# Kernel tuning notes

Measured on AMD Instinct MI355X. Metric: run time of the kernel, lower is better.

## Reference

```python
import jax, jax.numpy as jnp
import numpy as np

NUM_EMBEDDINGS = 512
EMBEDDING_DIM = 256
COMMITMENT_COST = 0.25


def setup_inputs() -> dict:
    key = jax.random.key(0)
    k1, k2 = jax.random.split(key)
    z = jax.random.normal(k1, (8, EMBEDDING_DIM, 16, 32, 32), dtype=jnp.float32)
    # codebook initialized uniform(-1/K, 1/K) like the torch module
    e = jax.random.uniform(k2, (NUM_EMBEDDINGS, EMBEDDING_DIM), dtype=jnp.float32,
                           minval=-1.0 / NUM_EMBEDDINGS, maxval=1.0 / NUM_EMBEDDINGS)
    return {"z": z, "e": e}


def reference(z, e):
    B, D, T, h, w = z.shape
    K = e.shape[0]
    # [B,D,T,h,w] -> [N, D]
    z_flat = jnp.transpose(z, (0, 2, 3, 4, 1)).reshape(-1, D)
    # squared L2 distances to codebook: [N, K]
    d = (jnp.sum(z_flat ** 2, axis=1, keepdims=True)
         + jnp.sum(e ** 2, axis=1)
         - 2.0 * z_flat @ e.T)
    idx = jnp.argmin(d, axis=1)                      # [N] int
    z_q_raw = e[idx].reshape(B, T, h, w, D)          # codebook gather
    z_q_raw = jnp.transpose(z_q_raw, (0, 4, 1, 2, 3))  # [B,D,T,h,w]

    commit = jnp.mean((jax.lax.stop_gradient(z_q_raw) - z) ** 2)
    codebk = jnp.mean((z_q_raw - jax.lax.stop_gradient(z)) ** 2)
    vq_loss = codebk + COMMITMENT_COST * commit

    # straight-through estimator
    z_q = z + jax.lax.stop_gradient(z_q_raw - z)

    # perplexity: histogram of code usage (avoids materializing NxK one-hot)
    N = idx.shape[0]
    avg_probs = jnp.zeros((K,), z.dtype).at[idx].add(1.0) / N
    perplexity = jnp.exp(-jnp.sum(avg_probs * jnp.log(avg_probs + 1e-10)))

    return z_q, vq_loss, idx, perplexity
```

## Files before the change

kernel.cpp:

```cpp
#include <hip/hip_runtime.h>
#include <math.h>

#define N_POS     131072
#define DIM       256
#define K_CODES   512
#define S_SPATIAL 16384
#define ZQ_ELEMS  33554432
#define OUT_LOSS  33554432
#define OUT_IDXB  33554433
#define OUT_PERP  (33554433 + 131072)

#define WS_LOSS   0
#define WS_HIST   16
#define WS_E2     2064
#define WS_FIXED  2064

__global__ __launch_bounds__(256) void e2_kernel(const float* __restrict__ e,
                                                 float* __restrict__ e2) {
    int k = blockIdx.x * 256 + threadIdx.x;
    if (k >= K_CODES) return;
    const float* row = e + (size_t)k * DIM;
    float half[2];
#pragma unroll
    for (int h = 0; h < 2; ++h) {
        const float* base = row + h * 128;
        float r[8];
#pragma unroll
        for (int j = 0; j < 8; ++j) {
            float v = base[j];
            r[j] = __fmul_rn(v, v);
        }
        for (int i = 8; i < 128; i += 8) {
#pragma unroll
            for (int j = 0; j < 8; ++j) {
                float v = base[i + j];
                r[j] = __fadd_rn(r[j], __fmul_rn(v, v));
            }
        }
        half[h] = __fadd_rn(__fadd_rn(__fadd_rn(r[0], r[1]), __fadd_rn(r[2], r[3])),
                            __fadd_rn(__fadd_rn(r[4], r[5]), __fadd_rn(r[6], r[7])));
    }
    e2[k] = __fadd_rn(half[0], half[1]);
}

__global__ __launch_bounds__(256) void transpose_e(const float* __restrict__ e,
                                                   float* __restrict__ eTq) {
    int t = blockIdx.x * 256 + threadIdx.x;
    int k = t >> 8;
    int d = t & 255;
    float v = e[t];
    int c = k >> 7;
    int w = (k >> 6) & 1;
    int l = k & 63;
    eTq[(((d << 1) + w) << 8) + (l << 2) + c] = v;
}

__global__ __launch_bounds__(256) void sz_kernel(const float* __restrict__ z,
                                                 float* __restrict__ sz) {
    int n = blockIdx.x * 256 + threadIdx.x;
    int b = n >> 14;
    int s = n & (S_SPATIAL - 1);
    const float* zp = z + (size_t)b * (DIM * S_SPATIAL) + s;
    float half[2];
#pragma unroll
    for (int h = 0; h < 2; ++h) {
        const float* base = zp + (size_t)(h * 128) * S_SPATIAL;
        float r[8];
#pragma unroll
        for (int j = 0; j < 8; ++j) {
            float v = base[(size_t)j * S_SPATIAL];
            r[j] = __fmul_rn(v, v);
        }
        for (int i = 8; i < 128; i += 8) {
#pragma unroll
            for (int j = 0; j < 8; ++j) {
                float v = base[(size_t)(i + j) * S_SPATIAL];
                r[j] = __fadd_rn(r[j], __fmul_rn(v, v));
            }
        }
        half[h] = __fadd_rn(__fadd_rn(__fadd_rn(r[0], r[1]), __fadd_rn(r[2], r[3])),
                            __fadd_rn(__fadd_rn(r[4], r[5]), __fadd_rn(r[6], r[7])));
    }
    sz[n] = __fadd_rn(half[0], half[1]);
}

__global__ __launch_bounds__(128, 4) void pass1_dist(const float* __restrict__ z,
                                                     const float* __restrict__ eTq,
                                                     const float* __restrict__ e2,
                                                     const float* __restrict__ sz,
                                                     float* __restrict__ idxf,
                                                     int* __restrict__ ghist) {
    const int lane = threadIdx.x & 63;
    const int wave = threadIdx.x >> 6;
    const int n0   = blockIdx.x << 4;
    const int b    = n0 >> 14;
    const float* zb = z + (size_t)b * (DIM * S_SPATIAL) + (n0 & (S_SPATIAL - 1));

    __shared__ float zs[DIM][16];
    __shared__ unsigned long long lred[2][16];

    for (int j = threadIdx.x; j < 1024; j += 128) {
        int d  = j >> 2;
        int p4 = (j & 3) << 2;
        float4 v = *(const float4*)(zb + ((size_t)d << 14) + p4);
        *(float4*)(&zs[d][p4]) = v;
    }

    float szv = sz[n0 + (lane & 15)];

    const int kbase = (wave << 6) + lane;
    float se0 = e2[kbase];
    float se1 = e2[kbase + 128];
    float se2 = e2[kbase + 256];
    float se3 = e2[kbase + 384];

    float a0[16], a1[16], a2[16], a3[16];
#pragma unroll
    for (int p = 0; p < 16; ++p) { a0[p] = 0.f; a1[p] = 0.f; a2[p] = 0.f; a3[p] = 0.f; }

    __syncthreads();

    const float* ep = eTq + (size_t)(((wave << 6) + lane) << 2);
#pragma unroll 2
    for (int d = 0; d < DIM; ++d) {
        float4 ev = *(const float4*)(ep + ((size_t)d << 9));
        float zv[16];
        *(float4*)(zv +  0) = *(const float4*)(&zs[d][ 0]);
        *(float4*)(zv +  4) = *(const float4*)(&zs[d][ 4]);
        *(float4*)(zv +  8) = *(const float4*)(&zs[d][ 8]);
        *(float4*)(zv + 12) = *(const float4*)(&zs[d][12]);
#pragma unroll
        for (int p = 0; p < 16; ++p) {
            a0[p] = __fmaf_rn(zv[p], ev.x, a0[p]);
            a1[p] = __fmaf_rn(zv[p], ev.y, a1[p]);
            a2[p] = __fmaf_rn(zv[p], ev.z, a2[p]);
            a3[p] = __fmaf_rn(zv[p], ev.w, a3[p]);
        }
    }

#pragma unroll
    for (int p = 0; p < 16; ++p) {
        float szp = __shfl(szv, p);
        float d0 = __fsub_rn(__fadd_rn(szp, se0), __fmul_rn(2.0f, a0[p]));
        float d1 = __fsub_rn(__fadd_rn(szp, se1), __fmul_rn(2.0f, a1[p]));
        float d2 = __fsub_rn(__fadd_rn(szp, se2), __fmul_rn(2.0f, a2[p]));
        float d3 = __fsub_rn(__fadd_rn(szp, se3), __fmul_rn(2.0f, a3[p]));
        unsigned long long k0 =
            ((unsigned long long)__float_as_uint(d0) << 32) | (unsigned int)(kbase);
        unsigned long long k1 =
            ((unsigned long long)__float_as_uint(d1) << 32) | (unsigned int)(kbase + 128);
        unsigned long long k2 =
            ((unsigned long long)__float_as_uint(d2) << 32) | (unsigned int)(kbase + 256);
        unsigned long long k3 =
            ((unsigned long long)__float_as_uint(d3) << 32) | (unsigned int)(kbase + 384);
        unsigned long long m01 = k1 < k0 ? k1 : k0;
        unsigned long long m23 = k3 < k2 ? k3 : k2;
        unsigned long long kmin = m23 < m01 ? m23 : m01;
#pragma unroll
        for (int off = 32; off; off >>= 1) {
            unsigned long long o = __shfl_xor(kmin, off);
            kmin = o < kmin ? o : kmin;
        }
        if (lane == 0) lred[wave][p] = kmin;
    }
    __syncthreads();
    if (threadIdx.x < 16) {
        int p = threadIdx.x;
        unsigned long long m = lred[0][p] < lred[1][p] ? lred[0][p] : lred[1][p];
        int idx = (int)(unsigned int)(m & 0xffffffffull);
        idxf[n0 + p] = (float)idx;
        atomicAdd(&ghist[idx], 1);
    }
}

__global__ __launch_bounds__(256) void gather_loss(const float* __restrict__ z,
                                                   const float* __restrict__ e,
                                                   const float* __restrict__ idxf,
                                                   float* __restrict__ out,
                                                   double* __restrict__ loss) {
    int t = blockIdx.x * 256 + threadIdx.x;
    int b   = t >> 14;
    int r   = t & 16383;
    int dg  = r >> 12;
    int sp  = (r & 4095) << 2;
    int n0  = (b << 14) + sp;

    int k0 = (int)idxf[n0 + 0];
    int k1 = (int)idxf[n0 + 1];
    int k2 = (int)idxf[n0 + 2];
    int k3 = (int)idxf[n0 + 3];
    const float* e0 = e + (size_t)k0 * DIM;
    const float* e1 = e + (size_t)k1 * DIM;
    const float* e2p = e + (size_t)k2 * DIM;
    const float* e3 = e + (size_t)k3 * DIM;

    const float* zb = z + ((size_t)b * DIM << 14) + sp;
    float* ob = out + ((size_t)b * DIM << 14) + sp;

    double acc = 0.0;
    int dend = dg * 64 + 64;
    for (int d0 = dg * 64; d0 < dend; d0 += 4) {
        float4 ev0 = *(const float4*)(e0 + d0);
        float4 ev1 = *(const float4*)(e1 + d0);
        float4 ev2 = *(const float4*)(e2p + d0);
        float4 ev3 = *(const float4*)(e3 + d0);
#pragma unroll
        for (int dd = 0; dd < 4; ++dd) {
            size_t off = ((size_t)(d0 + dd) << 14);
            float4 zv = *(const float4*)(zb + off);
            float ea = (dd == 0) ? ev0.x : (dd == 1) ? ev0.y : (dd == 2) ? ev0.z : ev0.w;
            float eb_ = (dd == 0) ? ev1.x : (dd == 1) ? ev1.y : (dd == 2) ? ev1.z : ev1.w;
            float ec = (dd == 0) ? ev2.x : (dd == 1) ? ev2.y : (dd == 2) ? ev2.z : ev2.w;
            float ed = (dd == 0) ? ev3.x : (dd == 1) ? ev3.y : (dd == 2) ? ev3.z : ev3.w;
            float d0f = __fsub_rn(ea, zv.x);
            float d1f = __fsub_rn(eb_, zv.y);
            float d2f = __fsub_rn(ec, zv.z);
            float d3f = __fsub_rn(ed, zv.w);
            float4 ov;
            ov.x = __fadd_rn(zv.x, d0f);
            ov.y = __fadd_rn(zv.y, d1f);
            ov.z = __fadd_rn(zv.z, d2f);
            ov.w = __fadd_rn(zv.w, d3f);
            *(float4*)(ob + off) = ov;
            acc += (double)d0f * (double)d0f;
            acc += (double)d1f * (double)d1f;
            acc += (double)d2f * (double)d2f;
            acc += (double)d3f * (double)d3f;
        }
    }
    for (int off = 32; off; off >>= 1) acc += __shfl_down(acc, off);
    __shared__ double red[4];
    if ((threadIdx.x & 63) == 0) red[threadIdx.x >> 6] = acc;
    __syncthreads();
    if (threadIdx.x == 0) {
        double tsum = red[0] + red[1] + red[2] + red[3];
        atomicAdd(loss, tsum);
    }
}

__global__ __launch_bounds__(512) void finalize_kernel(const int* __restrict__ ghist,
                                                       const double* __restrict__ loss,
                                                       float* __restrict__ out) {
    int k = threadIdx.x;
    double p = (double)ghist[k] / (double)N_POS;
    double t = p * log(p + 1e-10);
    for (int off = 32; off; off >>= 1) t += __shfl_down(t, off);
    __shared__ double red[8];
    if ((k & 63) == 0) red[k >> 6] = t;
    __syncthreads();
    if (k == 0) {
        double sum = 0.0;
        for (int i = 0; i < 8; ++i) sum += red[i];
        double perp = exp(-sum);
        double mse  = (*loss) / (double)ZQ_ELEMS;
        out[OUT_LOSS] = (float)(1.25 * mse);
        out[OUT_PERP] = (float)perp;
    }
}

extern "C" void kernel_launch(void* const* d_in, const int* in_sizes, int n_in,
                              void* d_out, int out_size, void* d_ws, size_t ws_size,
                              hipStream_t stream) {
    const float* z = (const float*)d_in[0];
    const float* e = (const float*)d_in[1];
    float* out = (float*)d_out;
    char* ws = (char*)d_ws;

    double* loss  = (double*)(ws + WS_LOSS);
    int*    ghist = (int*)(ws + WS_HIST);
    float*  e2    = (float*)(ws + WS_E2);
    float*  idxf  = out + OUT_IDXB;

    float* eTq = (float*)d_out;
    float* szp = (float*)d_out + 131072;

    hipMemsetAsync(d_ws, 0, WS_FIXED, stream);

    e2_kernel      <<<2, 256, 0, stream>>>(e, e2);
    transpose_e    <<<512, 256, 0, stream>>>(e, eTq);
    sz_kernel      <<<N_POS / 256, 256, 0, stream>>>(z, szp);
    pass1_dist     <<<N_POS / 16, 128, 0, stream>>>(z, eTq, e2, szp, idxf, ghist);
    gather_loss    <<<N_POS / 256, 256, 0, stream>>>(z, e, idxf, out, loss);
    finalize_kernel<<<1, 512, 0, stream>>>(ghist, loss, out);
}
```

Baseline: 685.3 us.

## Use one wave per 16-position tile with 8 codes per lane and double-buffered loads

The distance kernel now runs a single 64-lane wave per block. Each lane accumulates 8 codes × 16 positions (128 accumulators) instead of 4 × 16, and the codebook transpose layout changes so each lane loads two contiguous float4s per dimension. The main loop is software double-buffered, with shared-memory z loads and global codebook loads issued one step ahead, and the cross-wave LDS reduction plus second barrier are removed. The intent is to halve shared-memory z traffic per FMA and hide load latency. The cost is much higher register pressure (launch bounds 64,2), which risks lower occupancy or spills.

```diff
diff --git a/kernel.cpp b/kernel.cpp
--- a/kernel.cpp
+++ b/kernel.cpp
@@ -49,10 +49,9 @@
     int k = t >> 8;
     int d = t & 255;
     float v = e[t];
-    int c = k >> 7;
-    int w = (k >> 6) & 1;
+    int c = k >> 6;
     int l = k & 63;
-    eTq[(((d << 1) + w) << 8) + (l << 2) + c] = v;
+    eTq[(d << 9) + (l << 3) + c] = v;
 }
 
 __global__ __launch_bounds__(256) void sz_kernel(const float* __restrict__ z,
@@ -84,22 +83,20 @@
     sz[n] = __fadd_rn(half[0], half[1]);
 }
 
-__global__ __launch_bounds__(128, 4) void pass1_dist(const float* __restrict__ z,
-                                                     const float* __restrict__ eTq,
-                                                     const float* __restrict__ e2,
-                                                     const float* __restrict__ sz,
-                                                     float* __restrict__ idxf,
-                                                     int* __restrict__ ghist) {
-    const int lane = threadIdx.x & 63;
-    const int wave = threadIdx.x >> 6;
+__global__ __launch_bounds__(64, 2) void pass1_dist(const float* __restrict__ z,
+                                                    const float* __restrict__ eTq,
+                                                    const float* __restrict__ e2,
+                                                    const float* __restrict__ sz,
+                                                    float* __restrict__ idxf,
+                                                    int* __restrict__ ghist) {
+    const int lane = threadIdx.x;
     const int n0   = blockIdx.x << 4;
     const int b    = n0 >> 14;
     const float* zb = z + (size_t)b * (DIM * S_SPATIAL) + (n0 & (S_SPATIAL - 1));
 
     __shared__ float zs[DIM][16];
-    __shared__ unsigned long long lred[2][16];
-
-    for (int j = threadIdx.x; j < 1024; j += 128) {
+
+    for (int j = lane; j < 1024; j += 64) {
         int d  = j >> 2;
         int p4 = (j & 3) << 2;
         float4 v = *(const float4*)(zb + ((size_t)d << 14) + p4);
@@ -108,67 +105,103 @@
 
     float szv = sz[n0 + (lane & 15)];
 
-    const int kbase = (wave << 6) + lane;
-    float se0 = e2[kbase];
-    float se1 = e2[kbase + 128];
-    float se2 = e2[kbase + 256];
-    float se3 = e2[kbase + 384];
-
-    float a0[16], a1[16], a2[16], a3[16];
-#pragma unroll
-    for (int p = 0; p < 16; ++p) { a0[p] = 0.f; a1[p] = 0.f; a2[p] = 0.f; a3[p] = 0.f; }
+    float se[8];
+#pragma unroll
+    for (int c = 0; c < 8; ++c) se[c] = e2[(c << 6) + lane];
+
+    float a0[16], a1[16], a2[16], a3[16], a4[16], a5[16], a6[16], a7[16];
+#pragma unroll
+    for (int p = 0; p < 16; ++p) {
+        a0[p] = 0.f; a1[p] = 0.f; a2[p] = 0.f; a3[p] = 0.f;
+        a4[p] = 0.f; a5[p] = 0.f; a6[p] = 0.f; a7[p] = 0.f;
+    }
 
     __syncthreads();
 
-    const float* ep = eTq + (size_t)(((wave << 6) + lane) << 2);
-#pragma unroll 2
-    for (int d = 0; d < DIM; ++d) {
-        float4 ev = *(const float4*)(ep + ((size_t)d << 9));
-        float zv[16];
-        *(float4*)(zv +  0) = *(const float4*)(&zs[d][ 0]);
-        *(float4*)(zv +  4) = *(const float4*)(&zs[d][ 4]);
-        *(float4*)(zv +  8) = *(const float4*)(&zs[d][ 8]);
-        *(float4*)(zv + 12) = *(const float4*)(&zs[d][12]);
-#pragma unroll
-        for (int p = 0; p < 16; ++p) {
-            a0[p] = __fmaf_rn(zv[p], ev.x, a0[p]);
-            a1[p] = __fmaf_rn(zv[p], ev.y, a1[p]);
-            a2[p] = __fmaf_rn(zv[p], ev.z, a2[p]);
-            a3[p] = __fmaf_rn(zv[p], ev.w, a3[p]);
-        }
-    }
-
+    const float* ep = eTq + (lane << 3);
+
+#define LOADZ(zv, d) do {                                        \
+        *(float4*)((zv) +  0) = *(const float4*)(&zs[(d)][ 0]);  \
+        *(float4*)((zv) +  4) = *(const float4*)(&zs[(d)][ 4]);  \
+        *(float4*)((zv) +  8) = *(const float4*)(&zs[(d)][ 8]);  \
+        *(float4*)((zv) + 12) = *(const float4*)(&zs[(d)][12]);  \
+    } while (0)
+
+#define LOADE(e0, e1, d) do {                                    \
+        e0 = *(const float4*)(ep + ((size_t)(d) << 9));          \
+        e1 = *(const float4*)(ep + ((size_t)(d) << 9) + 4);      \
+    } while (0)
+
+#define FMAS(zv, e0, e1) do {                                    \
+        _Pragma("unroll")                                        \
+        for (int p = 0; p < 16; ++p) {                           \
+            float zp_ = (zv)[p];                                 \
+            a0[p] = __fmaf_rn(zp_, (e0).x, a0[p]);               \
+            a1[p] = __fmaf_rn(zp_, (e0).y, a1[p]);               \
+            a2[p] = __fmaf_rn(zp_, (e0).z, a2[p]);               \
+            a3[p] = __fmaf_rn(zp_, (e0).w, a3[p]);               \
+            a4[p] = __fmaf_rn(zp_, (e1).x, a4[p]);               \
+            a5[p] = __fmaf_rn(zp_, (e1).y, a5[p]);               \
+            a6[p] = __fmaf_rn(zp_, (e1).z, a6[p]);               \
+            a7[p] = __fmaf_rn(zp_, (e1).w, a7[p]);               \
+        }                                                        \
+    } while (0)
+
+    float zvA[16], zvB[16];
+    float4 eA0, eA1, eB0, eB1;
+    LOADZ(zvA, 0); LOADE(eA0, eA1, 0);
+    LOADZ(zvB, 1); LOADE(eB0, eB1, 1);
+#pragma unroll 1
+    for (int d = 0; d < DIM - 2; d += 2) {
+        FMAS(zvA, eA0, eA1);
+        LOADZ(zvA, d + 2); LOADE(eA0, eA1, d + 2);
+        FMAS(zvB, eB0, eB1);
+        LOADZ(zvB, d + 3); LOADE(eB0, eB1, d + 3);
+    }
+    FMAS(zvA, eA0, eA1);
+    FMAS(zvB, eB0, eB1);
+
+#undef LOADZ
+#undef LOADE
+#undef FMAS
+
+    unsigned long long myMin = 0xffffffffffffffffull;
 #pragma unroll
     for (int p = 0; p < 16; ++p) {
         float szp = __shfl(szv, p);
-        float d0 = __fsub_rn(__fadd_rn(szp, se0), __fmul_rn(2.0f, a0[p]));
-        float d1 = __fsub_rn(__fadd_rn(szp, se1), __fmul_rn(2.0f, a1[p]));
-        float d2 = __fsub_rn(__fadd_rn(szp, se2), __fmul_rn(2.0f, a2[p]));
-        float d3 = __fsub_rn(__fadd_rn(szp, se3), __fmul_rn(2.0f, a3[p]));
-        unsigned long long k0 =
-            ((unsigned long long)__float_as_uint(d0) << 32) | (unsigned int)(kbase);
-        unsigned long long k1 =
-            ((unsigned long long)__float_as_uint(d1) << 32) | (unsigned int)(kbase + 128);
-        unsigned long long k2 =
-            ((unsigned long long)__float_as_uint(d2) << 32) | (unsigned int)(kbase + 256);
-        unsigned long long k3 =
-            ((unsigned long long)__float_as_uint(d3) << 32) | (unsigned int)(kbase + 384);
+        float d0 = __fsub_rn(__fadd_rn(szp, se[0]), __fmul_rn(2.0f, a0[p]));
+        float d1 = __fsub_rn(__fadd_rn(szp, se[1]), __fmul_rn(2.0f, a1[p]));
+        float d2 = __fsub_rn(__fadd_rn(szp, se[2]), __fmul_rn(2.0f, a2[p]));
+        float d3 = __fsub_rn(__fadd_rn(szp, se[3]), __fmul_rn(2.0f, a3[p]));
+        float d4 = __fsub_rn(__fadd_rn(szp, se[4]), __fmul_rn(2.0f, a4[p]));
+        float d5 = __fsub_rn(__fadd_rn(szp, se[5]), __fmul_rn(2.0f, a5[p]));
+        float d6 = __fsub_rn(__fadd_rn(szp, se[6]), __fmul_rn(2.0f, a6[p]));
+        float d7 = __fsub_rn(__fadd_rn(szp, se[7]), __fmul_rn(2.0f, a7[p]));
+        unsigned long long k0 = ((unsigned long long)__float_as_uint(d0) << 32) | (unsigned int)(lane);
+        unsigned long long k1 = ((unsigned long long)__float_as_uint(d1) << 32) | (unsigned int)(lane + 64);
+        unsigned long long k2 = ((unsigned long long)__float_as_uint(d2) << 32) | (unsigned int)(lane + 128);
+        unsigned long long k3 = ((unsigned long long)__float_as_uint(d3) << 32) | (unsigned int)(lane + 192);
+        unsigned long long k4 = ((unsigned long long)__float_as_uint(d4) << 32) | (unsigned int)(lane + 256);
+        unsigned long long k5 = ((unsigned long long)__float_as_uint(d5) << 32) | (unsigned int)(lane + 320);
+        unsigned long long k6 = ((unsigned long long)__float_as_uint(d6) << 32) | (unsigned int)(lane + 384);
+        unsigned long long k7 = ((unsigned long long)__float_as_uint(d7) << 32) | (unsigned int)(lane + 448);
         unsigned long long m01 = k1 < k0 ? k1 : k0;
         unsigned long long m23 = k3 < k2 ? k3 : k2;
-        unsigned long long kmin = m23 < m01 ? m23 : m01;
+        unsigned long long m45 = k5 < k4 ? k5 : k4;
+        unsigned long long m67 = k7 < k6 ? k7 : k6;
+        unsigned long long mA = m23 < m01 ? m23 : m01;
+        unsigned long long mB = m67 < m45 ? m67 : m45;
+        unsigned long long kmin = mB < mA ? mB : mA;
 #pragma unroll
         for (int off = 32; off; off >>= 1) {
             unsigned long long o = __shfl_xor(kmin, off);
             kmin = o < kmin ? o : kmin;
         }
-        if (lane == 0) lred[wave][p] = kmin;
-    }
-    __syncthreads();
-    if (threadIdx.x < 16) {
-        int p = threadIdx.x;
-        unsigned long long m = lred[0][p] < lred[1][p] ? lred[0][p] : lred[1][p];
-        int idx = (int)(unsigned int)(m & 0xffffffffull);
-        idxf[n0 + p] = (float)idx;
+        if (lane == p) myMin = kmin;
+    }
+    if (lane < 16) {
+        int idx = (int)(unsigned int)(myMin & 0xffffffffull);
+        idxf[n0 + lane] = (float)idx;
         atomicAdd(&ghist[idx], 1);
     }
 }
@@ -279,7 +312,7 @@
     e2_kernel      <<<2, 256, 0, stream>>>(e, e2);
     transpose_e    <<<512, 256, 0, stream>>>(e, eTq);
     sz_kernel      <<<N_POS / 256, 256, 0, stream>>>(z, szp);
-    pass1_dist     <<<N_POS / 16, 128, 0, stream>>>(z, eTq, e2, szp, idxf, ghist);
+    pass1_dist     <<<N_POS / 16, 64, 0, stream>>>(z, eTq, e2, szp, idxf, ghist);
     gather_loss    <<<N_POS / 256, 256, 0, stream>>>(z, e, idxf, out, loss);
     finalize_kernel<<<1, 512, 0, stream>>>(ghist, loss, out);
 }
```

Result: no change. 677.1 us (-1.2%).
